# Optimization experiments

Hardware: AMD Instinct MI355X
Metric: run time of the kernel (lower is better)

## Reference

```python
import jax, jax.numpy as jnp
import numpy as np

B, H, W, C = 4, 256, 256, 64
KH = KW = 3
UNITS = 1          # forced: conv in-channels must equal kernel in-channels (see notes)
G = 1              # num_deformable_group
HP, WP = H + 2, W + 2  # 'same' padding for 3x3 stride-1: pad 1 each side


def _conv_indices(h, w):
    """Replicates tf.image.extract_image_patches('SAME') on an index grid:
    border patches read zero-padded coordinates. Returns int [h, w, 9]."""
    yg, xg = jnp.meshgrid(jnp.arange(h), jnp.arange(w), indexing='ij')
    yp = jnp.pad(yg, 1)
    xp = jnp.pad(xg, 1)
    ys = jnp.stack([yp[ky:ky + h, kx:kx + w] for ky in range(KH) for kx in range(KW)], -1)
    xs = jnp.stack([xp[ky:ky + h, kx:kx + w] for ky in range(KH) for kx in range(KW)], -1)
    return ys, xs


def setup_inputs() -> dict:
    key = jax.random.key(0)
    k1, k2, k3, k4 = jax.random.split(key, 4)
    input_fp = jax.random.normal(k1, (B, H, W, C), jnp.float32)
    gt_mask = jax.random.randint(k2, (1, H, W, 1), 0, 2).astype(jnp.float32)
    offset = jax.random.normal(k3, (B, H, W, UNITS * KH * KW * 2), jnp.float32)
    fan_in = KH * KW * C
    kernel = jax.random.normal(k4, (KH, KW, C, UNITS), jnp.float32) / np.float32(np.sqrt(fan_in))
    bias = jnp.zeros((UNITS,), jnp.float32)
    return {"input_fp": input_fp, "gt_mask": gt_mask, "offset": offset,
            "kernel": kernel, "bias": bias}


def reference(input_fp, gt_mask, offset, kernel, bias):
    pad = ((0, 0), (1, 1), (1, 1), (0, 0))
    fp = jnp.pad(input_fp, pad)                 # [B, HP, WP, C]
    mk = jnp.pad(gt_mask, pad)[0, :, :, 0]      # [HP, WP]; original tiles this over batch/channels

    off = offset.reshape(B, H, W, UNITS * KH * KW, 2)
    y_off, x_off = off[..., 0], off[..., 1]     # [B, H, W, 9]

    yi, xi = _conv_indices(H, W)                # [H, W, 9] int
    yf = yi[None].astype(jnp.float32)           # [1, H, W, 9], broadcasts over batch
    xf = xi[None].astype(jnp.float32)

    # mask at base sample points and at offset sample points
    p_mask = mk[yi, xi][None]                                        # [1, H, W, 9]
    yo = jnp.clip(jnp.floor(yf + y_off).astype(jnp.int32), 0, HP - 1)
    xo = jnp.clip(jnp.floor(xf + x_off).astype(jnp.int32), 0, WP - 1)
    p_mask_off = mk[yo, xo]                                          # [B, H, W, 9]
    diff = (p_mask != p_mask_off).astype(jnp.float32)

    y = jnp.clip(yf + y_off * diff, 0.0, H - 1.0)
    x = jnp.clip(xf + x_off * diff, 0.0, W - 1.0)
    y0 = jnp.floor(y).astype(jnp.int32)
    x0 = jnp.floor(x).astype(jnp.int32)

    b = jnp.arange(B)[:, None, None, None]
    pixels = fp[b, y0, x0]                      # [B, H, W, 9, C] nearest-floor sampling
    # [B,H,W,kh,kw,G,C] -> [B,H,kh,W,kw,G,C] -> [B, H*kh, W*kw, G*C]
    pixels = pixels.reshape(B, H, W, KH, KW, G, C)
    pixels = pixels.transpose(0, 1, 3, 2, 4, 5, 6)
    pixels = pixels.reshape(B, H * KH, W * KW, G * C)   # feat_in_group = units//G = 1, tile is a no-op

    out = jax.lax.conv_general_dilated(
        pixels, kernel, window_strides=(KH, KW), padding='SAME',
        dimension_numbers=('NHWC', 'HWIO', 'NHWC'))      # [B, H, W, UNITS]
    return out + bias
```

## Files before the change

kernel.cpp:

```cpp
#include <hip/hip_runtime.h>

#define HW 256
#define CH 64
#define NPIX (4 * HW * HW)
#define ENC_BYTES ((size_t)NPIX * 24)
#define DM_OFF ((size_t)8 << 20)
#define DM_BYTES ((size_t)NPIX * 48)
#define WS_NEED (DM_OFF + DM_BYTES)

__global__ __launch_bounds__(256, 8) void DeformA_kernel(
    const float* __restrict__ gt,
    const float* __restrict__ off,
    unsigned short* __restrict__ enc)
{
    const unsigned g = blockIdx.x * 256u + threadIdx.x;
    const unsigned p = g / 9u;
    const int tap = (int)(g - p * 9u);
    const int i = (int)((p >> 8) & 255u);
    const int j = (int)(p & 255u);
    const int ky = tap / 3, kx = tap - ky * 3;

    const float2 o2 = *(const float2*)(off + (size_t)g * 2);

    const int iy = i + ky - 1, ix = j + kx - 1;
    const bool interior = (iy >= 0) & (iy < HW) & (ix >= 0) & (ix < HW);
    const int yi = interior ? iy : 0;
    const int xi = interior ? ix : 0;
    const float p_mask = (yi >= 1 && xi >= 1) ? gt[(yi - 1) * HW + (xi - 1)] : 0.f;

    const float yf = (float)yi, xf = (float)xi;
    const float yof = fminf(fmaxf(floorf(yf + o2.x), 0.f), 257.f);
    const float xof = fminf(fmaxf(floorf(xf + o2.y), 0.f), 257.f);
    const int yo = (int)yof, xo = (int)xof;
    const float p_mask_off = (yo >= 1 && yo <= HW && xo >= 1 && xo <= HW)
                             ? gt[(yo - 1) * HW + (xo - 1)] : 0.f;
    const float diff = (p_mask != p_mask_off) ? 1.f : 0.f;
    const float y = fminf(fmaxf(yf + o2.x * diff, 0.f), 255.f);
    const float x = fminf(fmaxf(xf + o2.y * diff, 0.f), 255.f);
    const int y0 = (int)y, x0 = (int)x;

    enc[p * 12u + (unsigned)tap] = (unsigned short)((y0 << 8) | x0);
}

__global__ __launch_bounds__(256, 8) void DeformD_kernel(
    const float* __restrict__ inp,
    const float* __restrict__ ker,
    float* __restrict__ dm)
{
    __shared__ float wlds[576];
    const int tid = threadIdx.x;
    if (tid < 144) ((float4*)wlds)[tid] = ((const float4*)ker)[tid];
    const float4* wq = (const float4*)wlds;

    const int lane = tid & 63;
    const int wave = tid >> 6;
    const int t = lane & 15;
    const int g = lane >> 4;

    const int p0 = blockIdx.x * 32 + (wave * 4 + g) * 2;

    const float4 v0 = *(const float4*)(inp + (size_t)p0 * 64 + t * 4);
    const float4 v1 = *(const float4*)(inp + (size_t)(p0 + 1) * 64 + t * 4);

    __syncthreads();

    float da[9], db[9];
    #pragma unroll
    for (int k = 0; k < 9; ++k) {
        const float4 w = wq[k * 16 + t];
        da[k] = v0.x * w.x + v0.y * w.y + v0.z * w.z + v0.w * w.w;
        db[k] = v1.x * w.x + v1.y * w.y + v1.z * w.z + v1.w * w.w;
    }
    #pragma unroll
    for (int k = 0; k < 9; ++k) {
        da[k] += __shfl_xor(da[k], 8);
        da[k] += __shfl_xor(da[k], 4);
        da[k] += __shfl_xor(da[k], 2);
        da[k] += __shfl_xor(da[k], 1);
        db[k] += __shfl_xor(db[k], 8);
        db[k] += __shfl_xor(db[k], 4);
        db[k] += __shfl_xor(db[k], 2);
        db[k] += __shfl_xor(db[k], 1);
    }
    float sa = da[8], sb = db[8];
    #pragma unroll
    for (int k = 7; k >= 0; --k) {
        sa = (t == k) ? da[k] : sa;
        sb = (t == k) ? db[k] : sb;
    }
    if (t < 9) {
        dm[(size_t)p0 * 12 + t] = sa;
        dm[(size_t)(p0 + 1) * 12 + t] = sb;
    }
}

__global__ __launch_bounds__(256, 8) void DeformC2_kernel(
    const unsigned short* __restrict__ enc,
    const float* __restrict__ dm,
    const float* __restrict__ bias,
    float* __restrict__ out)
{
    const int tid = threadIdx.x;
    const int bid = blockIdx.x;
    const int vb = (bid & 7) * 128 + (bid >> 3);
    const int p = vb * 256 + tid;
    const int b = p >> 16;
    const float* dmb = dm + (size_t)(b << 16) * 12;

    const uint2* e = (const uint2*)(enc + (size_t)p * 12u);
    const uint2 eA = e[0];
    const uint2 eB = e[1];
    const unsigned eC = *(const unsigned*)(e + 2);

    unsigned en[9];
    en[0] = eA.x & 0xffffu; en[1] = eA.x >> 16;
    en[2] = eA.y & 0xffffu; en[3] = eA.y >> 16;
    en[4] = eB.x & 0xffffu; en[5] = eB.x >> 16;
    en[6] = eB.y & 0xffffu; en[7] = eB.y >> 16;
    en[8] = eC & 0xffffu;

    float v[9];
    int msk = 0;
    #pragma unroll
    for (int k = 0; k < 9; ++k) {
        const int yy = (int)(en[k] >> 8);
        const int xx = (int)(en[k] & 255u);
        const bool valid = (yy >= 1) & (xx >= 1);
        msk |= (int)valid << k;
        const int idx = valid ? ((yy - 1) * HW + (xx - 1)) : 0;
        v[k] = dmb[(size_t)idx * 12 + k];
    }
    float sum = 0.f;
    #pragma unroll
    for (int k = 0; k < 9; ++k)
        sum += ((msk >> k) & 1) ? v[k] : 0.f;

    out[p] = sum + bias[0];
}

__global__ __launch_bounds__(256, 6) void DeformFallback_kernel(
    const float* __restrict__ inp, const float* __restrict__ gt,
    const float* __restrict__ off, const float* __restrict__ ker,
    const float* __restrict__ bias, float* __restrict__ out)
{
    __shared__ float wlds[576];
    const int tid = threadIdx.x;
    if (tid < 144) ((float4*)wlds)[tid] = ((const float4*)ker)[tid];

    const int lane = tid & 63;
    const int wave = tid >> 6;
    const int q16  = lane & 48;
    const int t    = lane & 15;

    const int bid = blockIdx.x;
    const int vb  = (bid & 7) * 2048 + (bid >> 3);

    const int p = vb * 16 + wave * 4 + (q16 >> 4);
    const int b = p >> 16;
    const int i = (p >> 8) & 255;
    const int j = p & 255;
    const float* inb = inp + (long)b * (HW * HW * CH);

    int pack = 0;
    if (t < 9) {
        const int tap = t;
        const int ky = tap / 3, kx = tap - ky * 3;
        int iy = i + ky - 1, ix = j + kx - 1;
        bool interior = (iy >= 0) & (iy < HW) & (ix >= 0) & (ix < HW);
        int yi = interior ? iy : 0;
        int xi = interior ? ix : 0;
        float p_mask = (yi >= 1 && xi >= 1) ? gt[(yi - 1) * HW + (xi - 1)] : 0.f;
        float2 o2 = *(const float2*)(off + (long)p * 18 + 2 * tap);
        float yf = (float)yi, xf = (float)xi;
        float yof = fminf(fmaxf(floorf(yf + o2.x), 0.f), 257.f);
        float xof = fminf(fmaxf(floorf(xf + o2.y), 0.f), 257.f);
        int yo = (int)yof, xo = (int)xof;
        float p_mask_off = (yo >= 1 && yo <= HW && xo >= 1 && xo <= HW)
                           ? gt[(yo - 1) * HW + (xo - 1)] : 0.f;
        float diff = (p_mask != p_mask_off) ? 1.f : 0.f;
        float y = fminf(fmaxf(yf + o2.x * diff, 0.f), 255.f);
        float x = fminf(fmaxf(xf + o2.y * diff, 0.f), 255.f);
        int y0 = (int)y;
        int x0 = (int)x;
        bool valid = (y0 >= 1) & (x0 >= 1);
        int eoff = ((y0 - 1) * HW + (x0 - 1)) * CH;
        pack = valid ? eoff : -1;
    }

    int pk[9];
    #pragma unroll
    for (int k = 0; k < 9; ++k) pk[k] = __shfl(pack, q16 + k);

    float4 v[9];
    #pragma unroll
    for (int k = 0; k < 9; ++k) {
        int eo2 = pk[k] >= 0 ? pk[k] : 0;
        v[k] = *(const float4*)(inb + eo2 + t * 4);
    }

    __syncthreads();

    float acc = 0.f;
    #pragma unroll
    for (int k = 0; k < 9; ++k) {
        float s = pk[k] >= 0 ? 1.f : 0.f;
        float4 w = ((const float4*)wlds)[k * 16 + t];
        float d = v[k].x * w.x + v[k].y * w.y + v[k].z * w.z + v[k].w * w.w;
        acc = fmaf(s, d, acc);
    }

    acc += __shfl_xor(acc, 8);
    acc += __shfl_xor(acc, 4);
    acc += __shfl_xor(acc, 2);
    acc += __shfl_xor(acc, 1);
    if (t == 0) out[p] = acc + bias[0];
}

extern "C" void kernel_launch(void* const* d_in, const int* in_sizes, int n_in,
                              void* d_out, int out_size, void* d_ws, size_t ws_size,
                              hipStream_t stream) {
    const float* inp  = (const float*)d_in[0];
    const float* gt   = (const float*)d_in[1];
    const float* off  = (const float*)d_in[2];
    const float* ker  = (const float*)d_in[3];
    const float* bias = (const float*)d_in[4];
    float* out = (float*)d_out;

    if (d_ws != nullptr && ws_size >= WS_NEED) {
        unsigned short* enc = (unsigned short*)d_ws;
        float* dm = (float*)((char*)d_ws + DM_OFF);
        DeformA_kernel<<<9216, 256, 0, stream>>>(gt, off, enc);
        DeformD_kernel<<<8192, 256, 0, stream>>>(inp, ker, dm);
        DeformC2_kernel<<<1024, 256, 0, stream>>>(enc, dm, bias, out);
    } else {
        DeformFallback_kernel<<<16384, 256, 0, stream>>>(inp, gt, off, ker, bias, out);
    }
}
```

Baseline: 138.8 us.

## Compute per-pixel tap dot products one thread per pixel instead of shuffle reductions

The precompute kernel that forms the 9 per-tap channel dot products for each pixel is restructured. Instead of 16 lanes sharing a pixel, doing partial dot products, reducing with cross-lane shuffles and selecting one result per lane, each thread now handles a whole pixel. It reads its 64 channels and accumulates all 9 taps serially, reading the weights straight from global memory (uniform, cache-friendly) rather than LDS, and writes three float4s. This removes the shuffle reduction and LDS staging, but each thread reads 256 contiguous bytes, so the input loads are strided across lanes and less coalesced, and register use rises.

```diff
diff --git a/kernel.cpp b/kernel.cpp
--- a/kernel.cpp
+++ b/kernel.cpp
@@ -42,56 +42,47 @@
     enc[p * 12u + (unsigned)tap] = (unsigned short)((y0 << 8) | x0);
 }
 
-__global__ __launch_bounds__(256, 8) void DeformD_kernel(
+__global__ __launch_bounds__(256, 4) void DeformD2_kernel(
     const float* __restrict__ inp,
     const float* __restrict__ ker,
     float* __restrict__ dm)
 {
-    __shared__ float wlds[576];
-    const int tid = threadIdx.x;
-    if (tid < 144) ((float4*)wlds)[tid] = ((const float4*)ker)[tid];
-    const float4* wq = (const float4*)wlds;
-
-    const int lane = tid & 63;
-    const int wave = tid >> 6;
-    const int t = lane & 15;
-    const int g = lane >> 4;
-
-    const int p0 = blockIdx.x * 32 + (wave * 4 + g) * 2;
-
-    const float4 v0 = *(const float4*)(inp + (size_t)p0 * 64 + t * 4);
-    const float4 v1 = *(const float4*)(inp + (size_t)(p0 + 1) * 64 + t * 4);
-
-    __syncthreads();
-
-    float da[9], db[9];
-    #pragma unroll
-    for (int k = 0; k < 9; ++k) {
-        const float4 w = wq[k * 16 + t];
-        da[k] = v0.x * w.x + v0.y * w.y + v0.z * w.z + v0.w * w.w;
-        db[k] = v1.x * w.x + v1.y * w.y + v1.z * w.z + v1.w * w.w;
-    }
-    #pragma unroll
-    for (int k = 0; k < 9; ++k) {
-        da[k] += __shfl_xor(da[k], 8);
-        da[k] += __shfl_xor(da[k], 4);
-        da[k] += __shfl_xor(da[k], 2);
-        da[k] += __shfl_xor(da[k], 1);
-        db[k] += __shfl_xor(db[k], 8);
-        db[k] += __shfl_xor(db[k], 4);
-        db[k] += __shfl_xor(db[k], 2);
-        db[k] += __shfl_xor(db[k], 1);
-    }
-    float sa = da[8], sb = db[8];
-    #pragma unroll
-    for (int k = 7; k >= 0; --k) {
-        sa = (t == k) ? da[k] : sa;
-        sb = (t == k) ? db[k] : sb;
-    }
-    if (t < 9) {
-        dm[(size_t)p0 * 12 + t] = sa;
-        dm[(size_t)(p0 + 1) * 12 + t] = sb;
-    }
+    const int p = blockIdx.x * 256 + threadIdx.x;
+    const float* ip = inp + (size_t)p * 64;
+
+    float acc[9];
+    #pragma unroll
+    for (int k = 0; k < 9; ++k) acc[k] = 0.f;
+
+    #pragma unroll
+    for (int c4 = 0; c4 < 4; ++c4) {
+        const float4 a = *(const float4*)(ip + c4 * 16 + 0);
+        const float4 b = *(const float4*)(ip + c4 * 16 + 4);
+        const float4 c = *(const float4*)(ip + c4 * 16 + 8);
+        const float4 d = *(const float4*)(ip + c4 * 16 + 12);
+        #pragma unroll
+        for (int k = 0; k < 9; ++k) {
+            const float* kr = ker + k * 64 + c4 * 16;
+            const float4 wa = *(const float4*)(kr + 0);
+            const float4 wb = *(const float4*)(kr + 4);
+            const float4 wc = *(const float4*)(kr + 8);
+            const float4 wd = *(const float4*)(kr + 12);
+            acc[k] = fmaf(a.x, wa.x, acc[k]); acc[k] = fmaf(a.y, wa.y, acc[k]);
+            acc[k] = fmaf(a.z, wa.z, acc[k]); acc[k] = fmaf(a.w, wa.w, acc[k]);
+            acc[k] = fmaf(b.x, wb.x, acc[k]); acc[k] = fmaf(b.y, wb.y, acc[k]);
+            acc[k] = fmaf(b.z, wb.z, acc[k]); acc[k] = fmaf(b.w, wb.w, acc[k]);
+            acc[k] = fmaf(c.x, wc.x, acc[k]); acc[k] = fmaf(c.y, wc.y, acc[k]);
+            acc[k] = fmaf(c.z, wc.z, acc[k]); acc[k] = fmaf(c.w, wc.w, acc[k]);
+            acc[k] = fmaf(d.x, wd.x, acc[k]); acc[k] = fmaf(d.y, wd.y, acc[k]);
+            acc[k] = fmaf(d.z, wd.z, acc[k]); acc[k] = fmaf(d.w, wd.w, acc[k]);
+        }
+    }
+
+    float4* o = (float4*)(dm + (size_t)p * 12);
+    const float4 s0 = {acc[0], acc[1], acc[2], acc[3]};
+    const float4 s1 = {acc[4], acc[5], acc[6], acc[7]};
+    const float4 s2 = {acc[8], 0.f, 0.f, 0.f};
+    o[0] = s0; o[1] = s1; o[2] = s2;
 }
 
 __global__ __launch_bounds__(256, 8) void DeformC2_kernel(
@@ -230,7 +221,7 @@
         unsigned short* enc = (unsigned short*)d_ws;
         float* dm = (float*)((char*)d_ws + DM_OFF);
         DeformA_kernel<<<9216, 256, 0, stream>>>(gt, off, enc);
-        DeformD_kernel<<<8192, 256, 0, stream>>>(inp, ker, dm);
+        DeformD2_kernel<<<1024, 256, 0, stream>>>(inp, ker, dm);
         DeformC2_kernel<<<1024, 256, 0, stream>>>(enc, dm, bias, out);
     } else {
         DeformFallback_kernel<<<16384, 256, 0, stream>>>(inp, gt, off, ker, bias, out);
```

After: 129.6 us. 1.07x faster.
